# Performance work log

Measured on AMD Instinct MI355X. Metric: run time of the kernel, lower is better.

The kernel has to match this reference:

```python
import jax, jax.numpy as jnp
import numpy as np

MARGIN = 0.1
REDUCTION = 'mean'  # 'mean' or 'sum'

def setup_inputs() -> dict:
    key = jax.random.key(0)
    k1, k2 = jax.random.split(key)
    B, N = 16384, 64
    scores = jax.random.normal(k1, (B * N,), dtype=jnp.float32)
    werRank = jax.random.randint(k2, (B, N), 0, N, dtype=jnp.int64)
    return {"scores": scores, "werRank": werRank, "n_best": N}

def reference(scores, werRank, n_best):
    B = werRank.shape[0]
    N = n_best
    s = scores.reshape(B, N)                      # [B, N] per-utterance n-best scores
    g = jnp.take_along_axis(s, werRank, axis=1)   # [B, N] scores ordered by WER rank (best first)
    # pairwise margin: d[b, i, j] = g[b, j] - g[b, i] + margin, for worse-ranked j > i
    d = g[:, None, :] - g[:, :, None] + MARGIN    # [B, N, N]
    upper = jnp.triu(jnp.ones((N, N), dtype=bool), k=1)  # j > i
    hinge = jnp.where(upper[None], jnp.maximum(d, 0.0), 0.0)
    per_i = hinge.sum(axis=2)                     # [B, N] sum over worse hypotheses j
    if REDUCTION == 'mean':
        counts = (N - 1) - jnp.arange(N)          # len(nBestRank[i+1:]) for each i
        denom = jnp.where(counts > 0, counts, 1).astype(per_i.dtype)
        per_i = per_i / denom[None, :]            # row i=N-1 contributes 0 (skipped in original)
    return per_i.sum()
```

## Files before the change

### kernel.cpp

```cpp
#include <hip/hip_runtime.h>

#define MARGIN 0.1f
#define NBEST 64
#define ROWS_PER_WAVE 8

__global__ __launch_bounds__(256)
void sml_kernel(const float* __restrict__ scores,
                const unsigned int* __restrict__ wr32,
                float* __restrict__ ws, int B)
{
    const int lane = threadIdx.x & 63;
    const int wib  = threadIdx.x >> 6;
    const int b0   = (blockIdx.x * 4 + wib) * ROWS_PER_WAVE;

    unsigned int probe = wr32[2 * lane + 1];
    const bool is64 = (__all(probe == 0u) != 0);

    unsigned int rk[ROWS_PER_WAVE];
    #pragma unroll
    for (int r = 0; r < ROWS_PER_WAVE; ++r) {
        int bc = min(b0 + r, B - 1);
        int idx = bc * NBEST + lane;
        rk[r] = is64 ? wr32[2 * idx] : wr32[idx];
    }
    float gv[ROWS_PER_WAVE];
    #pragma unroll
    for (int r = 0; r < ROWS_PER_WAVE; ++r) {
        int bc = min(b0 + r, B - 1);
        gv[r] = scores[bc * NBEST + (int)(rk[r] & (NBEST - 1))];
    }

    float t[ROWS_PER_WAVE], a[ROWS_PER_WAVE];
    #pragma unroll
    for (int r = 0; r < ROWS_PER_WAVE; ++r) {
        t[r] = MARGIN - gv[r];
        a[r] = 0.0f;
    }

    #pragma unroll
    for (int c = 1; c < NBEST; ++c) {
        float m01 = (lane < c) ? 1.0f : 0.0f;
        #pragma unroll
        for (int r = 0; r < ROWS_PER_WAVE; ++r) {
            float s = __uint_as_float(
                __builtin_amdgcn_readlane(__float_as_uint(gv[r]), c));
            a[r] += fmaxf(s + t[r], 0.0f) * m01;
        }
    }

    float accs = 0.0f;
    #pragma unroll
    for (int r = 0; r < ROWS_PER_WAVE; ++r)
        accs += (b0 + r < B) ? a[r] : 0.0f;
    int cnt = (NBEST - 1) - lane;
    float acc = accs / (float)(cnt > 0 ? cnt : 1);

    #pragma unroll
    for (int off = 32; off > 0; off >>= 1)
        acc += __shfl_down(acc, off);

    __shared__ float wsum[4];
    if (lane == 0) wsum[wib] = acc;
    __syncthreads();
    if (threadIdx.x == 0)
        ws[blockIdx.x] = wsum[0] + wsum[1] + wsum[2] + wsum[3];
}

__global__ __launch_bounds__(256)
void sml_reduce(const float* __restrict__ ws, float* __restrict__ out, int n)
{
    const int lane = threadIdx.x & 63;
    const int wid  = threadIdx.x >> 6;
    float s = 0.0f;
    for (int i = threadIdx.x; i < n; i += 256) s += ws[i];
    #pragma unroll
    for (int off = 32; off > 0; off >>= 1)
        s += __shfl_down(s, off);
    __shared__ float wsum[4];
    if (lane == 0) wsum[wid] = s;
    __syncthreads();
    if (threadIdx.x == 0)
        out[0] = wsum[0] + wsum[1] + wsum[2] + wsum[3];
}

extern "C" void kernel_launch(void* const* d_in, const int* in_sizes, int n_in,
                              void* d_out, int out_size, void* d_ws, size_t ws_size,
                              hipStream_t stream)
{
    const float* scores    = (const float*)d_in[0];
    const unsigned int* wr = (const unsigned int*)d_in[1];
    const int B = in_sizes[0] / NBEST;

    const int rows_per_block = 4 * ROWS_PER_WAVE;
    const int blocks = (B + rows_per_block - 1) / rows_per_block;
    sml_kernel<<<blocks, 256, 0, stream>>>(scores, wr, (float*)d_ws, B);
    sml_reduce<<<1, 256, 0, stream>>>((const float*)d_ws, (float*)d_out, blocks);
}
```

Before: 16.12 us.

## Fuse final reduction via last-block atomics and broadcast scores through LDS

The separate reduction launch is replaced by a two-level atomic counter scheme inside the main kernel. The last block to finish sums the per-block partials, which removes a second kernel launch. The inner pairwise loop now reads rank-ordered scores (plus margin) as float4 broadcasts from shared memory instead of using per-element readlane. It also uses the identity max(g_c+m, g_i) - g_i, folding the subtraction into one fma at the end. The counters live in the workspace and rely on modulo wraparound across calls, so their correctness depends on their initial state. The fused path only applies when the block count fits the power-of-two grouping.

```diff
diff --git a/kernel.cpp b/kernel.cpp
--- a/kernel.cpp
+++ b/kernel.cpp
@@ -2,68 +2,122 @@
 
 #define MARGIN 0.1f
 #define NBEST 64
-#define ROWS_PER_WAVE 8
+#define RPW 8
+#define GRP 8
+
+#define CNT1_OFF (16384 / 4)
+#define CNT1_STRIDE 16
+#define CNT2_OFF (CNT1_OFF + 64 * CNT1_STRIDE + CNT1_STRIDE)
 
 __global__ __launch_bounds__(256)
 void sml_kernel(const float* __restrict__ scores,
                 const unsigned int* __restrict__ wr32,
-                float* __restrict__ ws, int B)
+                float* __restrict__ ws, float* __restrict__ out,
+                int B, int lastblock)
 {
     const int lane = threadIdx.x & 63;
     const int wib  = threadIdx.x >> 6;
-    const int b0   = (blockIdx.x * 4 + wib) * ROWS_PER_WAVE;
+    const int b0   = (blockIdx.x * 4 + wib) * RPW;
 
     unsigned int probe = wr32[2 * lane + 1];
     const bool is64 = (__all(probe == 0u) != 0);
 
-    unsigned int rk[ROWS_PER_WAVE];
+    unsigned int rk[RPW];
     #pragma unroll
-    for (int r = 0; r < ROWS_PER_WAVE; ++r) {
-        int bc = min(b0 + r, B - 1);
-        int idx = bc * NBEST + lane;
-        rk[r] = is64 ? wr32[2 * idx] : wr32[idx];
+    for (int r = 0; r < RPW; ++r) {
+        int bc  = min(b0 + r, B - 1);
+        rk[r] = is64 ? wr32[2 * (bc * NBEST + lane)] : wr32[bc * NBEST + lane];
     }
-    float gv[ROWS_PER_WAVE];
+    float gv[RPW];
     #pragma unroll
-    for (int r = 0; r < ROWS_PER_WAVE; ++r) {
+    for (int r = 0; r < RPW; ++r) {
         int bc = min(b0 + r, B - 1);
         gv[r] = scores[bc * NBEST + (int)(rk[r] & (NBEST - 1))];
     }
 
-    float t[ROWS_PER_WAVE], a[ROWS_PER_WAVE];
+    __shared__ float4 q4[4][2][NBEST];
+    q4[wib][0][lane] = make_float4(gv[0] + MARGIN, gv[1] + MARGIN,
+                                   gv[2] + MARGIN, gv[3] + MARGIN);
+    q4[wib][1][lane] = make_float4(gv[4] + MARGIN, gv[5] + MARGIN,
+                                   gv[6] + MARGIN, gv[7] + MARGIN);
+
+    float acc[RPW];
     #pragma unroll
-    for (int r = 0; r < ROWS_PER_WAVE; ++r) {
-        t[r] = MARGIN - gv[r];
-        a[r] = 0.0f;
-    }
+    for (int r = 0; r < RPW; ++r) acc[r] = 0.0f;
+
+    __syncthreads();
 
     #pragma unroll
     for (int c = 1; c < NBEST; ++c) {
-        float m01 = (lane < c) ? 1.0f : 0.0f;
-        #pragma unroll
-        for (int r = 0; r < ROWS_PER_WAVE; ++r) {
-            float s = __uint_as_float(
-                __builtin_amdgcn_readlane(__float_as_uint(gv[r]), c));
-            a[r] += fmaxf(s + t[r], 0.0f) * m01;
-        }
+        float4 qa = q4[wib][0][c];
+        float4 qb = q4[wib][1][c];
+        float mm = (lane < c) ? 1.0f : 0.0f;
+        acc[0] = fmaf(fmaxf(qa.x, gv[0]), mm, acc[0]);
+        acc[1] = fmaf(fmaxf(qa.y, gv[1]), mm, acc[1]);
+        acc[2] = fmaf(fmaxf(qa.z, gv[2]), mm, acc[2]);
+        acc[3] = fmaf(fmaxf(qa.w, gv[3]), mm, acc[3]);
+        acc[4] = fmaf(fmaxf(qb.x, gv[4]), mm, acc[4]);
+        acc[5] = fmaf(fmaxf(qb.y, gv[5]), mm, acc[5]);
+        acc[6] = fmaf(fmaxf(qb.z, gv[6]), mm, acc[6]);
+        acc[7] = fmaf(fmaxf(qb.w, gv[7]), mm, acc[7]);
     }
 
+    const float cntf = (float)((NBEST - 1) - lane);
     float accs = 0.0f;
     #pragma unroll
-    for (int r = 0; r < ROWS_PER_WAVE; ++r)
-        accs += (b0 + r < B) ? a[r] : 0.0f;
+    for (int r = 0; r < RPW; ++r) {
+        float ar = fmaf(-gv[r], cntf, acc[r]);
+        accs += (b0 + r < B) ? ar : 0.0f;
+    }
     int cnt = (NBEST - 1) - lane;
-    float acc = accs / (float)(cnt > 0 ? cnt : 1);
+    float accv = accs / (float)(cnt > 0 ? cnt : 1);
 
     #pragma unroll
     for (int off = 32; off > 0; off >>= 1)
-        acc += __shfl_down(acc, off);
+        accv += __shfl_down(accv, off);
 
     __shared__ float wsum[4];
-    if (lane == 0) wsum[wib] = acc;
+    if (lane == 0) wsum[wib] = accv;
     __syncthreads();
-    if (threadIdx.x == 0)
+
+    if (!lastblock) {
+        if (threadIdx.x == 0)
+            ws[blockIdx.x] = wsum[0] + wsum[1] + wsum[2] + wsum[3];
+        return;
+    }
+
+    __shared__ int amlast;
+    if (threadIdx.x == 0) {
         ws[blockIdx.x] = wsum[0] + wsum[1] + wsum[2] + wsum[3];
+        __threadfence();
+        unsigned int* cnt1 = (unsigned int*)ws + CNT1_OFF;
+        unsigned int* cnt2 = (unsigned int*)ws + CNT2_OFF;
+        unsigned g = (unsigned)blockIdx.x / GRP;
+        unsigned o1 = atomicAdd(&cnt1[g * CNT1_STRIDE], 1u);
+        int last = 0;
+        if (((o1 + 1u) & (GRP - 1u)) == 0u) {
+            __threadfence();
+            unsigned o2 = atomicAdd(cnt2, 1u);
+            unsigned ngroups = gridDim.x / GRP;
+            last = (((o2 + 1u) & (ngroups - 1u)) == 0u);
+        }
+        amlast = last;
+    }
+    __syncthreads();
+    if (amlast) {
+        __threadfence();
+        const int n = gridDim.x;
+        float s = 0.0f;
+        for (int i = threadIdx.x; i < n; i += 256) s += ws[i];
+        #pragma unroll
+        for (int off = 32; off > 0; off >>= 1)
+            s += __shfl_down(s, off);
+        __shared__ float w2[4];
+        if (lane == 0) w2[wib] = s;
+        __syncthreads();
+        if (threadIdx.x == 0)
+            out[0] = w2[0] + w2[1] + w2[2] + w2[3];
+    }
 }
 
 __global__ __launch_bounds__(256)
@@ -91,8 +145,14 @@
     const unsigned int* wr = (const unsigned int*)d_in[1];
     const int B = in_sizes[0] / NBEST;
 
-    const int rows_per_block = 4 * ROWS_PER_WAVE;
+    const int rows_per_block = 4 * RPW;
     const int blocks = (B + rows_per_block - 1) / rows_per_block;
-    sml_kernel<<<blocks, 256, 0, stream>>>(scores, wr, (float*)d_ws, B);
-    sml_reduce<<<1, 256, 0, stream>>>((const float*)d_ws, (float*)d_out, blocks);
+    const int ngroups = blocks / GRP;
+    const bool single = (blocks % GRP == 0) && ((ngroups & (ngroups - 1)) == 0);
+
+    sml_kernel<<<blocks, 256, 0, stream>>>(scores, wr, (float*)d_ws,
+                                           (float*)d_out, B, single ? 1 : 0);
+    if (!single)
+        sml_reduce<<<1, 256, 0, stream>>>((const float*)d_ws, (float*)d_out,
+                                          blocks);
 }
```

New measurement: 21.60 us. 1.34x slower.
